# Performance work log

Hardware: AMD Instinct MI355X
Metric: run time of the kernel (lower is better)

## Reference

```python
import jax, jax.numpy as jnp
import numpy as np

EPS = 1e-5

def _gcn_norm(edge_index, n):
    # Add self-loops, compute symmetric normalization deg^-1/2 * deg^-1/2 (PyG GCNConv).
    src = jnp.concatenate([edge_index[0], jnp.arange(n)])
    dst = jnp.concatenate([edge_index[1], jnp.arange(n)])
    deg = jax.ops.segment_sum(jnp.ones_like(dst, dtype=jnp.float32), dst, num_segments=n)
    dinv = jnp.where(deg > 0, jax.lax.rsqrt(deg), 0.0)
    norm = dinv[src] * dinv[dst]  # [E + N]
    return src, dst, norm

def _gcn_conv(x, W, b, src, dst, norm, n):
    h = x @ W                      # linear first (out_dim < in_dim here)
    msg = h[src] * norm[:, None]   # gather + per-edge scale
    out = jax.ops.segment_sum(msg, dst, num_segments=n)  # scatter-add aggregation
    return out + b

def _bn(x, g, b):
    # BatchNorm over nodes (training-mode batch statistics, biased variance)
    mu = x.mean(axis=0)
    var = jnp.mean((x - mu) ** 2, axis=0)
    return (x - mu) * jax.lax.rsqrt(var + EPS) * g + b


def setup_inputs() -> dict:
    key = jax.random.key(0)
    N, E, F_in = 10000, 320000, 256
    ks = jax.random.split(key, 8)
    dims = [F_in, 220, 150, 100, 60, 17]
    inp = {
        'x': jax.random.normal(ks[0], (N, F_in), dtype=jnp.float32),
        'edge_index': jax.random.randint(ks[1], (2, E), 0, N, dtype=jnp.int64),
    }
    for i in range(5):
        fan_in, fan_out = dims[i], dims[i + 1]
        scale = 1.0 / np.sqrt(fan_in)
        inp[f'W{i+1}'] = jax.random.normal(ks[2 + i], (fan_in, fan_out), dtype=jnp.float32) * scale
        inp[f'b{i+1}'] = jnp.zeros((fan_out,), dtype=jnp.float32)
    for i, d in enumerate([220, 150, 100, 60]):
        inp[f'g{i+1}'] = jnp.ones((d,), dtype=jnp.float32)
        inp[f'be{i+1}'] = jnp.zeros((d,), dtype=jnp.float32)
    return inp


def reference(x, edge_index, W1, b1, W2, b2, W3, b3, W4, b4, W5, b5,
              g1, be1, g2, be2, g3, be3, g4, be4):
    n = x.shape[0]
    src, dst, norm = _gcn_norm(edge_index, n)
    h = _gcn_conv(x, W1, b1, src, dst, norm, n)
    h = _bn(jax.nn.relu(h), g1, be1)
    # dropout omitted (eval-mode identity)
    h = _gcn_conv(h, W2, b2, src, dst, norm, n)
    h = _bn(jax.nn.relu(h), g2, be2)
    h = _gcn_conv(h, W3, b3, src, dst, norm, n)
    h = _bn(jax.nn.relu(h), g3, be3)
    h = _gcn_conv(h, W4, b4, src, dst, norm, n)
    h = _bn(jax.nn.relu(h), g4, be4)
    h = _gcn_conv(h, W5, b5, src, dst, norm, n)
    return jax.nn.log_softmax(h, axis=1)
```

## Files before the change

kernel.cpp:

```cpp
#include <hip/hip_runtime.h>
#include <math.h>

typedef unsigned short ushort_t;
typedef unsigned int uint_t;
typedef unsigned long long ull_t;

__device__ __forceinline__ float bf2f(ushort_t u) {
    union { uint_t i; float f; } x; x.i = ((uint_t)u) << 16; return x.f;
}
__device__ __forceinline__ ushort_t f2bf(float f) {
    union { float f; uint_t i; } x; x.f = f;
    uint_t r = x.i + 0x7FFFu + ((x.i >> 16) & 1u);
    return (ushort_t)(r >> 16);
}

__global__ __launch_bounds__(256) void k_init(
    int* __restrict__ cnt, float* __restrict__ stats, float* __restrict__ wbias, int N)
{
    const int gt = blockIdx.x * 256 + threadIdx.x;
    const int gth = gridDim.x * 256;
    for (int i = gt; i < N; i += gth) cnt[i] = 0;
    for (int i = gt; i < 2048; i += gth) stats[i] = 0.f;
    if (gt < 256) wbias[gt] = 0.f;
}

__global__ __launch_bounds__(256) void k_prep0(
    const float* __restrict__ W0, ushort_t* __restrict__ Wt)
{
    const int gt = blockIdx.x * 256 + threadIdx.x;
    const int gth = gridDim.x * 256;
    for (int idx = gt; idx < 224 * 256; idx += gth) {
        int j = idx >> 8;
        int k = idx & 255;
        float v = (j < 220) ? W0[(long)k * 220 + j] : 0.f;
        Wt[idx] = f2bf(v);
    }
}

__global__ void k_hist(const int* __restrict__ dst, int* __restrict__ cnt, int E) {
    int e = blockIdx.x * blockDim.x + threadIdx.x;
    if (e < E) atomicAdd(&cnt[dst[e]], 1);
}

__global__ __launch_bounds__(1024) void k_scan(
    const int* __restrict__ cnt, int* __restrict__ row_start,
    int* __restrict__ cursor, float* __restrict__ dinv, int N)
{
    __shared__ int sh[1024];
    const int tid = threadIdx.x;
    const int chunk = (N + 1023) >> 10;
    int loc[16];
    const int base = tid * chunk;
    int sum = 0;
    for (int c = 0; c < chunk; ++c) {
        int i = base + c;
        int v = (i < N) ? cnt[i] : 0;
        loc[c] = sum;
        sum += v;
    }
    sh[tid] = sum;
    __syncthreads();
    for (int off = 1; off < 1024; off <<= 1) {
        int v = (tid >= off) ? sh[tid - off] : 0;
        __syncthreads();
        sh[tid] += v;
        __syncthreads();
    }
    const int excl = sh[tid] - sum;
    for (int c = 0; c < chunk; ++c) {
        int i = base + c;
        if (i < N) {
            int rs = excl + loc[c];
            row_start[i] = rs;
            cursor[i] = rs;
            dinv[i] = rsqrtf(1.0f + (float)cnt[i]);
        }
    }
    if (tid == 1023) row_start[N] = sh[1023];
}

__global__ void k_fill(const int* __restrict__ src, const int* __restrict__ dst,
                       int* __restrict__ cursor, int* __restrict__ csr_src, int E) {
    int e = blockIdx.x * blockDim.x + threadIdx.x;
    if (e < E) {
        int pos = atomicAdd(&cursor[dst[e]], 1);
        csr_src[pos] = src[e];
    }
}

__global__ void k_prep(const float* __restrict__ W,
                       const float* __restrict__ g, const float* __restrict__ be,
                       const float* __restrict__ cs, const float* __restrict__ cq,
                       ushort_t* __restrict__ Wt, float* __restrict__ wbias,
                       int K, int M, int Kp, int Mp, int yW, float invN)
{
    __shared__ float sm[256];
    if ((int)blockIdx.y < yW) {
        if (threadIdx.y == 0) {
            int kk = blockIdx.x * 64 + threadIdx.x;
            float sc = 0.f;
            if (kk < K) {
                float mu = cs[kk] * invN;
                float var = cq[kk] * invN - mu * mu;
                sc = g[kk] * rsqrtf(var + 1e-5f);
            }
            sm[threadIdx.x] = sc;
        }
        __syncthreads();
        int k = blockIdx.x * 64 + threadIdx.x;
        int j = blockIdx.y * 4 + threadIdx.y;
        if (k >= Kp || j >= Mp) return;
        float v = 0.f;
        if (k < K && j < M) v = sm[threadIdx.x] * W[(long)k * M + j];
        Wt[(long)j * Kp + k] = f2bf(v);
    } else {
        __shared__ float red[4][64];
        int t = threadIdx.y * 64 + threadIdx.x;
        for (int kk = t; kk < K; kk += 256) {
            float mu = cs[kk] * invN;
            float var = cq[kk] * invN - mu * mu;
            float sc = g[kk] * rsqrtf(var + 1e-5f);
            sm[kk] = be[kk] - mu * sc;
        }
        __syncthreads();
        int jl = t & 63, kg = t >> 6;
        int j = blockIdx.x * 64 + jl;
        float s = 0.f;
        if (j < M) {
            for (int k = kg; k < K; k += 4) s += sm[k] * W[(long)k * M + j];
        }
        red[kg][jl] = s;
        __syncthreads();
        if (kg == 0 && j < Mp) wbias[j] = red[0][jl] + red[1][jl] + red[2][jl] + red[3][jl];
    }
}

template<int KP, bool F32A>
__global__ __launch_bounds__(256) void k_gemm_mfma(
    const void* __restrict__ Xin, const ushort_t* __restrict__ Wt,
    const float* __restrict__ wbias, const float* __restrict__ dinv,
    ushort_t* __restrict__ h2, int N, int Mp)
{
    typedef __attribute__((ext_vector_type(8))) short short8;
    typedef __attribute__((ext_vector_type(4))) float floatx4;
    constexpr int LSTR = KP + 16;
    __shared__ ushort_t Bs[64 * LSTR];

    const int tid = threadIdx.x;
    const int wave = tid >> 6, lane = tid & 63;
    const int m = lane & 15, quad = lane >> 4;
    const int i0 = blockIdx.x * 64 + wave * 16;
    const int j0 = blockIdx.y * 64;
    const int ncols = min(64, Mp - j0);
    const int ntiles = ncols >> 4;

    {
        const int cpr = KP / 8;
        const int chunks = ncols * cpr;
        for (int c = tid; c < chunks; c += 256) {
            int jj = c / cpr;
            int kk = (c - jj * cpr) * 8;
            *(short8*)(Bs + jj * LSTR + kk) =
                *(const short8*)(Wt + (long)(j0 + jj) * KP + kk);
        }
    }
    __syncthreads();

    if (i0 >= N) return;

    floatx4 acc[4];
    #pragma unroll
    for (int t = 0; t < 4; ++t) { acc[t].x = 0.f; acc[t].y = 0.f; acc[t].z = 0.f; acc[t].w = 0.f; }

    const int ra = min(i0 + m, N - 1);
    const ushort_t* arow_h = F32A ? nullptr : (const ushort_t*)Xin + (long)ra * KP + quad * 8;
    const float*    arow_f = F32A ? (const float*)Xin + (long)ra * KP + quad * 8 : nullptr;

    #pragma unroll
    for (int k0 = 0; k0 < KP; k0 += 32) {
        short8 av;
        if (F32A) {
            float4 f0 = *(const float4*)(arow_f + k0);
            float4 f1 = *(const float4*)(arow_f + k0 + 4);
            av[0] = (short)f2bf(f0.x); av[1] = (short)f2bf(f0.y);
            av[2] = (short)f2bf(f0.z); av[3] = (short)f2bf(f0.w);
            av[4] = (short)f2bf(f1.x); av[5] = (short)f2bf(f1.y);
            av[6] = (short)f2bf(f1.z); av[7] = (short)f2bf(f1.w);
        } else {
            av = *(const short8*)(arow_h + k0);
        }
        #pragma unroll
        for (int t = 0; t < 4; ++t) {
            if (t < ntiles) {
                short8 bv = *(const short8*)(Bs + (t * 16 + m) * LSTR + k0 + quad * 8);
                acc[t] = __builtin_amdgcn_mfma_f32_16x16x32_bf16(av, bv, acc[t], 0, 0, 0);
            }
        }
    }

    #pragma unroll
    for (int t = 0; t < 4; ++t) {
        if (t < ntiles) {
            int j = j0 + t * 16 + m;
            float wb = wbias[j];
            #pragma unroll
            for (int r = 0; r < 4; ++r) {
                int i = i0 + quad * 4 + r;
                if (i < N) h2[(long)i * Mp + j] = f2bf((acc[t][r] + wb) * dinv[i]);
            }
        }
    }
}

__global__ __launch_bounds__(256) void k_agg(
    const int* __restrict__ row_start, const int* __restrict__ csr_src,
    const ushort_t* __restrict__ h2, int hs,
    const float* __restrict__ dinv, const float* __restrict__ b,
    ushort_t* __restrict__ tmpb, int ts,
    int N, int M, int Q, ull_t magic, uint_t sh)
{
    const uint_t g = blockIdx.x * 256 + threadIdx.x;
    const uint_t i = (uint_t)(((ull_t)g * magic) >> sh);
    const int jp = (int)(g - i * Q);
    if (i >= (uint_t)N) return;
    const int j0 = jp * 8;
    if (j0 >= M) {
        *(uint4*)(tmpb + (long)i * ts + j0) = make_uint4(0u, 0u, 0u, 0u);
        return;
    }
    const int s0 = row_start[i];
    const int s1 = row_start[i + 1];
    const ushort_t* hp = h2 + j0;
    float acc[8];
    {
        uint4 v = *(const uint4*)(hp + (long)i * hs);
        acc[0] = bf2f((ushort_t)(v.x & 0xffff)); acc[1] = bf2f((ushort_t)(v.x >> 16));
        acc[2] = bf2f((ushort_t)(v.y & 0xffff)); acc[3] = bf2f((ushort_t)(v.y >> 16));
        acc[4] = bf2f((ushort_t)(v.z & 0xffff)); acc[5] = bf2f((ushort_t)(v.z >> 16));
        acc[6] = bf2f((ushort_t)(v.w & 0xffff)); acc[7] = bf2f((ushort_t)(v.w >> 16));
    }
    int e = s0;
    for (; e + 3 < s1; e += 4) {
        int n0 = csr_src[e], n1 = csr_src[e + 1], n2 = csr_src[e + 2], n3 = csr_src[e + 3];
        uint4 w0 = *(const uint4*)(hp + (long)n0 * hs);
        uint4 w1 = *(const uint4*)(hp + (long)n1 * hs);
        uint4 w2 = *(const uint4*)(hp + (long)n2 * hs);
        uint4 w3 = *(const uint4*)(hp + (long)n3 * hs);
        acc[0] += bf2f((ushort_t)(w0.x & 0xffff)); acc[1] += bf2f((ushort_t)(w0.x >> 16));
        acc[2] += bf2f((ushort_t)(w0.y & 0xffff)); acc[3] += bf2f((ushort_t)(w0.y >> 16));
        acc[4] += bf2f((ushort_t)(w0.z & 0xffff)); acc[5] += bf2f((ushort_t)(w0.z >> 16));
        acc[6] += bf2f((ushort_t)(w0.w & 0xffff)); acc[7] += bf2f((ushort_t)(w0.w >> 16));
        acc[0] += bf2f((ushort_t)(w1.x & 0xffff)); acc[1] += bf2f((ushort_t)(w1.x >> 16));
        acc[2] += bf2f((ushort_t)(w1.y & 0xffff)); acc[3] += bf2f((ushort_t)(w1.y >> 16));
        acc[4] += bf2f((ushort_t)(w1.z & 0xffff)); acc[5] += bf2f((ushort_t)(w1.z >> 16));
        acc[6] += bf2f((ushort_t)(w1.w & 0xffff)); acc[7] += bf2f((ushort_t)(w1.w >> 16));
        acc[0] += bf2f((ushort_t)(w2.x & 0xffff)); acc[1] += bf2f((ushort_t)(w2.x >> 16));
        acc[2] += bf2f((ushort_t)(w2.y & 0xffff)); acc[3] += bf2f((ushort_t)(w2.y >> 16));
        acc[4] += bf2f((ushort_t)(w2.z & 0xffff)); acc[5] += bf2f((ushort_t)(w2.z >> 16));
        acc[6] += bf2f((ushort_t)(w2.w & 0xffff)); acc[7] += bf2f((ushort_t)(w2.w >> 16));
        acc[0] += bf2f((ushort_t)(w3.x & 0xffff)); acc[1] += bf2f((ushort_t)(w3.x >> 16));
        acc[2] += bf2f((ushort_t)(w3.y & 0xffff)); acc[3] += bf2f((ushort_t)(w3.y >> 16));
        acc[4] += bf2f((ushort_t)(w3.z & 0xffff)); acc[5] += bf2f((ushort_t)(w3.z >> 16));
        acc[6] += bf2f((ushort_t)(w3.w & 0xffff)); acc[7] += bf2f((ushort_t)(w3.w >> 16));
    }
    for (; e < s1; ++e) {
        uint4 w = *(const uint4*)(hp + (long)csr_src[e] * hs);
        acc[0] += bf2f((ushort_t)(w.x & 0xffff)); acc[1] += bf2f((ushort_t)(w.x >> 16));
        acc[2] += bf2f((ushort_t)(w.y & 0xffff)); acc[3] += bf2f((ushort_t)(w.y >> 16));
        acc[4] += bf2f((ushort_t)(w.z & 0xffff)); acc[5] += bf2f((ushort_t)(w.z >> 16));
        acc[6] += bf2f((ushort_t)(w.w & 0xffff)); acc[7] += bf2f((ushort_t)(w.w >> 16));
    }
    const float di = dinv[i];
    ushort_t r[8];
    #pragma unroll
    for (int u = 0; u < 8; ++u) {
        float v = (j0 + u < M) ? fmaxf(acc[u] * di + b[j0 + u], 0.f) : 0.f;
        r[u] = f2bf(v);
    }
    uint4 pk;
    pk.x = (uint_t)r[0] | ((uint_t)r[1] << 16);
    pk.y = (uint_t)r[2] | ((uint_t)r[3] << 16);
    pk.z = (uint_t)r[4] | ((uint_t)r[5] << 16);
    pk.w = (uint_t)r[6] | ((uint_t)r[7] << 16);
    *(uint4*)(tmpb + (long)i * ts + j0) = pk;
}

__global__ __launch_bounds__(256) void k_stats(
    const ushort_t* __restrict__ tmpb, int ts,
    float* __restrict__ cs, float* __restrict__ csq, int N)
{
    const int t = threadIdx.x;
    if (2 * t >= ts) return;
    const int i0 = blockIdx.x * 64;
    float s0 = 0.f, q0 = 0.f, s1 = 0.f, q1 = 0.f;
    for (int r = 0; r < 64; ++r) {
        int i = i0 + r;
        if (i < N) {
            uint_t w = *(const uint_t*)(tmpb + (long)i * ts + 2 * t);
            float v0 = bf2f((ushort_t)(w & 0xffff));
            float v1 = bf2f((ushort_t)(w >> 16));
            s0 += v0; q0 += v0 * v0;
            s1 += v1; q1 += v1 * v1;
        }
    }
    atomicAdd(&cs[2 * t], s0);
    atomicAdd(&csq[2 * t], q0);
    atomicAdd(&cs[2 * t + 1], s1);
    atomicAdd(&csq[2 * t + 1], q1);
}

__global__ __launch_bounds__(256) void k_agg_final(
    const int* __restrict__ row_start, const int* __restrict__ csr_src,
    const ushort_t* __restrict__ h2, const float* __restrict__ dinv,
    const float* __restrict__ b, float* __restrict__ out, int N, int M)
{
    const int x = threadIdx.x;
    const int i = blockIdx.x * 16 + threadIdx.y;
    if (i >= N) return;
    const int j0 = 2 * x, j1 = 2 * x + 1;
    uint_t v = *(const uint_t*)(h2 + (long)i * 32 + j0);
    float a0 = bf2f((ushort_t)(v & 0xffff));
    float a1 = bf2f((ushort_t)(v >> 16));
    const int s0 = row_start[i];
    const int s1 = row_start[i + 1];
    int e = s0;
    for (; e + 1 < s1; e += 2) {
        int n0 = csr_src[e], n1 = csr_src[e + 1];
        uint_t w0 = *(const uint_t*)(h2 + (long)n0 * 32 + j0);
        uint_t w1 = *(const uint_t*)(h2 + (long)n1 * 32 + j0);
        a0 += bf2f((ushort_t)(w0 & 0xffff)); a1 += bf2f((ushort_t)(w0 >> 16));
        a0 += bf2f((ushort_t)(w1 & 0xffff)); a1 += bf2f((ushort_t)(w1 >> 16));
    }
    for (; e < s1; ++e) {
        uint_t w = *(const uint_t*)(h2 + (long)csr_src[e] * 32 + j0);
        a0 += bf2f((ushort_t)(w & 0xffff)); a1 += bf2f((ushort_t)(w >> 16));
    }
    const float di = dinv[i];
    float r0 = (j0 < M) ? (a0 * di + b[j0]) : -INFINITY;
    float r1 = (j1 < M) ? (a1 * di + b[j1]) : -INFINITY;
    float m = fmaxf(r0, r1);
    #pragma unroll
    for (int msk = 1; msk < 16; msk <<= 1) m = fmaxf(m, __shfl_xor(m, msk, 16));
    float s = ((j0 < M) ? expf(r0 - m) : 0.f) + ((j1 < M) ? expf(r1 - m) : 0.f);
    #pragma unroll
    for (int msk = 1; msk < 16; msk <<= 1) s += __shfl_xor(s, msk, 16);
    const float l = logf(s) + m;
    if (j0 < M) out[(long)i * M + j0] = r0 - l;
    if (j1 < M) out[(long)i * M + j1] = r1 - l;
}


static inline int pad16(int v) { return (v + 15) & ~15; }
static inline int pad32(int v) { return (v + 31) & ~31; }

extern "C" void kernel_launch(void* const* d_in, const int* in_sizes, int n_in,
                              void* d_out, int out_size, void* d_ws, size_t ws_size,
                              hipStream_t stream)
{
    const int dims[6] = {256, 220, 150, 100, 60, 17};
    const int N = in_sizes[0] / dims[0];
    const int E = in_sizes[1] / 2;

    const float* x  = (const float*)d_in[0];
    const int* ei   = (const int*)d_in[1];
    const int* srcv = ei;
    const int* dstv = ei + E;
    const float* Wl[5], *bl[5];
    for (int l = 0; l < 5; ++l) {
        Wl[l] = (const float*)d_in[2 + 2 * l];
        bl[l] = (const float*)d_in[3 + 2 * l];
    }
    const float* gl[4], *bel[4];
    for (int l = 0; l < 4; ++l) {
        gl[l]  = (const float*)d_in[12 + 2 * l];
        bel[l] = (const float*)d_in[13 + 2 * l];
    }
    float* out = (float*)d_out;

    char* w = (char*)d_ws;
    const long NB  = ((long)N * 4 + 255) & ~255L;
    const long NB1 = ((long)(N + 1) * 4 + 255) & ~255L;
    const long EB  = ((long)E * 4 + 255) & ~255L;
    const long FBB = ((long)N * 224 * 2 + 255) & ~255L;
    const long WTB = ((long)224 * 256 * 2 + 255) & ~255L;

    long o = 0;
    float* dinv      = (float*)(w + o);  o += NB;
    float* stats     = (float*)(w + o);  o += 2048 * 4;
    float* wbias     = (float*)(w + o);  o += 1024;
    int*   cnt       = (int*)(w + o);    o += NB;
    int*   row_start = (int*)(w + o);    o += NB1;
    int*   cursor    = (int*)(w + o);    o += NB;
    int*   csr_src   = (int*)(w + o);    o += EB;
    ushort_t* Wt     = (ushort_t*)(w + o); o += WTB;
    ushort_t* h2     = (ushort_t*)(w + o); o += FBB;
    ushort_t* tmpb   = (ushort_t*)(w + o); o += FBB;

    const int eBlk = (E + 255) / 256;
    const float invN = 1.0f / (float)N;

    k_init<<<(N + 255) / 256, 256, 0, stream>>>(cnt, stats, wbias, N);
    k_prep0<<<56, 256, 0, stream>>>(Wl[0], Wt);
    k_hist<<<eBlk, 256, 0, stream>>>(dstv, cnt, E);
    k_scan<<<1, 1024, 0, stream>>>(cnt, row_start, cursor, dinv, N);
    k_fill<<<eBlk, 256, 0, stream>>>(srcv, dstv, cursor, csr_src, E);

    for (int l = 0; l < 5; ++l) {
        const int K  = dims[l];
        const int M  = dims[l + 1];
        const int Kp = pad32(K);
        const int Mp = pad16(M);
        const int ts = (l < 4) ? pad32(M) : 32;

        if (l > 0) {
            const int yW = (Mp + 3) / 4;
            k_prep<<<dim3((Kp + 63) / 64, yW + 1), dim3(64, 4), 0, stream>>>(
                Wl[l], gl[l - 1], bel[l - 1],
                stats + (l - 1) * 512, stats + (l - 1) * 512 + 256,
                Wt, wbias, K, M, Kp, Mp, yW, invN);
        }

        dim3 gg((N + 63) / 64, (Mp + 63) / 64);
        if (l == 0) {
            k_gemm_mfma<256, true><<<gg, 256, 0, stream>>>(x, Wt, wbias, dinv, h2, N, Mp);
        } else {
            switch (Kp) {
                case 224: k_gemm_mfma<224, false><<<gg, 256, 0, stream>>>(tmpb, Wt, wbias, dinv, h2, N, Mp); break;
                case 160: k_gemm_mfma<160, false><<<gg, 256, 0, stream>>>(tmpb, Wt, wbias, dinv, h2, N, Mp); break;
                case 128: k_gemm_mfma<128, false><<<gg, 256, 0, stream>>>(tmpb, Wt, wbias, dinv, h2, N, Mp); break;
                case  64: k_gemm_mfma< 64, false><<<gg, 256, 0, stream>>>(tmpb, Wt, wbias, dinv, h2, N, Mp); break;
            }
        }

        if (l < 4) {
            const int Q = ts / 8;
            uint_t shmt = 0;
            while ((1u << shmt) < (uint_t)Q) ++shmt;
            shmt += 32;
            const ull_t magic = ((1ULL << shmt) + Q - 1) / (ull_t)Q;
            const long total = (long)N * Q;
            k_agg<<<(int)((total + 255) / 256), 256, 0, stream>>>(
                row_start, csr_src, h2, Mp, dinv, bl[l], tmpb, ts, N, M, Q, magic, shmt);
            k_stats<<<(N + 63) / 64, 256, 0, stream>>>(tmpb, ts,
                stats + l * 512, stats + l * 512 + 256, N);
        } else {
            k_agg_final<<<(N + 15) / 16, dim3(16, 16), 0, stream>>>(
                row_start, csr_src, h2, dinv, bl[l], out, N, M);
        }
    }
}
```

Baseline: 402.6 us.

## Fuse histogram with weight prep, CSR fill into GEMM, stats into aggregation

Merges the degree histogram and first-layer weight transpose into one launch. It runs the CSR fill in extra blocks of the layer-0 GEMM launch and accumulates batch-norm sums inside the aggregation kernel via shared-memory atomics. This removes several kernel launches and a re-read of the aggregated activations. In exchange it adds shared and global atomic traffic per block and computes stats from unrounded fp32 values.

```diff
diff --git a/kernel.cpp b/kernel.cpp
--- a/kernel.cpp
+++ b/kernel.cpp
@@ -24,22 +24,22 @@
     if (gt < 256) wbias[gt] = 0.f;
 }
 
-__global__ __launch_bounds__(256) void k_prep0(
+__global__ __launch_bounds__(256) void k_hist_prep0(
+    const int* __restrict__ dst, int* __restrict__ cnt, int E, int eBlk,
     const float* __restrict__ W0, ushort_t* __restrict__ Wt)
 {
-    const int gt = blockIdx.x * 256 + threadIdx.x;
-    const int gth = gridDim.x * 256;
-    for (int idx = gt; idx < 224 * 256; idx += gth) {
-        int j = idx >> 8;
-        int k = idx & 255;
-        float v = (j < 220) ? W0[(long)k * 220 + j] : 0.f;
-        Wt[idx] = f2bf(v);
-    }
-}
-
-__global__ void k_hist(const int* __restrict__ dst, int* __restrict__ cnt, int E) {
-    int e = blockIdx.x * blockDim.x + threadIdx.x;
-    if (e < E) atomicAdd(&cnt[dst[e]], 1);
+    if ((int)blockIdx.x < eBlk) {
+        int e = blockIdx.x * 256 + threadIdx.x;
+        if (e < E) atomicAdd(&cnt[dst[e]], 1);
+    } else {
+        int base = ((int)blockIdx.x - eBlk) * 256 + (int)threadIdx.x;
+        for (int idx = base; idx < 224 * 256; idx += 56 * 256) {
+            int j = idx >> 8;
+            int k = idx & 255;
+            float v = (j < 220) ? W0[(long)k * 220 + j] : 0.f;
+            Wt[idx] = f2bf(v);
+        }
+    }
 }
 
 __global__ __launch_bounds__(1024) void k_scan(
@@ -77,15 +77,6 @@
         }
     }
     if (tid == 1023) row_start[N] = sh[1023];
-}
-
-__global__ void k_fill(const int* __restrict__ src, const int* __restrict__ dst,
-                       int* __restrict__ cursor, int* __restrict__ csr_src, int E) {
-    int e = blockIdx.x * blockDim.x + threadIdx.x;
-    if (e < E) {
-        int pos = atomicAdd(&cursor[dst[e]], 1);
-        csr_src[pos] = src[e];
-    }
 }
 
 __global__ void k_prep(const float* __restrict__ W,
@@ -135,16 +126,30 @@
     }
 }
 
-template<int KP, bool F32A>
+template<int KP, bool F32A, bool FILL>
 __global__ __launch_bounds__(256) void k_gemm_mfma(
     const void* __restrict__ Xin, const ushort_t* __restrict__ Wt,
     const float* __restrict__ wbias, const float* __restrict__ dinv,
-    ushort_t* __restrict__ h2, int N, int Mp)
+    ushort_t* __restrict__ h2, int N, int Mp,
+    int gx, const int* __restrict__ fsrc, const int* __restrict__ fdst,
+    int* __restrict__ fcursor, int* __restrict__ fcsr, int fE)
 {
     typedef __attribute__((ext_vector_type(8))) short short8;
     typedef __attribute__((ext_vector_type(4))) float floatx4;
     constexpr int LSTR = KP + 16;
     __shared__ ushort_t Bs[64 * LSTR];
+
+    if (FILL) {
+        if ((int)blockIdx.x >= gx) {
+            const int fid = ((int)blockIdx.x - gx) * (int)gridDim.y + (int)blockIdx.y;
+            const int e = fid * 256 + (int)threadIdx.x;
+            if (e < fE) {
+                int pos = atomicAdd(&fcursor[fdst[e]], 1);
+                fcsr[pos] = fsrc[e];
+            }
+            return;
+        }
+    }
 
     const int tid = threadIdx.x;
     const int wave = tid >> 6, lane = tid & 63;
@@ -217,96 +222,99 @@
     const ushort_t* __restrict__ h2, int hs,
     const float* __restrict__ dinv, const float* __restrict__ b,
     ushort_t* __restrict__ tmpb, int ts,
+    float* __restrict__ cs, float* __restrict__ csq,
     int N, int M, int Q, ull_t magic, uint_t sh)
 {
-    const uint_t g = blockIdx.x * 256 + threadIdx.x;
+    __shared__ float s_s[256];
+    __shared__ float s_q[256];
+    const int tid = threadIdx.x;
+    s_s[tid] = 0.f;
+    s_q[tid] = 0.f;
+    __syncthreads();
+
+    const uint_t g = blockIdx.x * 256 + tid;
     const uint_t i = (uint_t)(((ull_t)g * magic) >> sh);
     const int jp = (int)(g - i * Q);
-    if (i >= (uint_t)N) return;
     const int j0 = jp * 8;
-    if (j0 >= M) {
-        *(uint4*)(tmpb + (long)i * ts + j0) = make_uint4(0u, 0u, 0u, 0u);
-        return;
-    }
-    const int s0 = row_start[i];
-    const int s1 = row_start[i + 1];
-    const ushort_t* hp = h2 + j0;
-    float acc[8];
-    {
-        uint4 v = *(const uint4*)(hp + (long)i * hs);
-        acc[0] = bf2f((ushort_t)(v.x & 0xffff)); acc[1] = bf2f((ushort_t)(v.x >> 16));
-        acc[2] = bf2f((ushort_t)(v.y & 0xffff)); acc[3] = bf2f((ushort_t)(v.y >> 16));
-        acc[4] = bf2f((ushort_t)(v.z & 0xffff)); acc[5] = bf2f((ushort_t)(v.z >> 16));
-        acc[6] = bf2f((ushort_t)(v.w & 0xffff)); acc[7] = bf2f((ushort_t)(v.w >> 16));
-    }
-    int e = s0;
-    for (; e + 3 < s1; e += 4) {
-        int n0 = csr_src[e], n1 = csr_src[e + 1], n2 = csr_src[e + 2], n3 = csr_src[e + 3];
-        uint4 w0 = *(const uint4*)(hp + (long)n0 * hs);
-        uint4 w1 = *(const uint4*)(hp + (long)n1 * hs);
-        uint4 w2 = *(const uint4*)(hp + (long)n2 * hs);
-        uint4 w3 = *(const uint4*)(hp + (long)n3 * hs);
-        acc[0] += bf2f((ushort_t)(w0.x & 0xffff)); acc[1] += bf2f((ushort_t)(w0.x >> 16));
-        acc[2] += bf2f((ushort_t)(w0.y & 0xffff)); acc[3] += bf2f((ushort_t)(w0.y >> 16));
-        acc[4] += bf2f((ushort_t)(w0.z & 0xffff)); acc[5] += bf2f((ushort_t)(w0.z >> 16));
-        acc[6] += bf2f((ushort_t)(w0.w & 0xffff)); acc[7] += bf2f((ushort_t)(w0.w >> 16));
-        acc[0] += bf2f((ushort_t)(w1.x & 0xffff)); acc[1] += bf2f((ushort_t)(w1.x >> 16));
-        acc[2] += bf2f((ushort_t)(w1.y & 0xffff)); acc[3] += bf2f((ushort_t)(w1.y >> 16));
-        acc[4] += bf2f((ushort_t)(w1.z & 0xffff)); acc[5] += bf2f((ushort_t)(w1.z >> 16));
-        acc[6] += bf2f((ushort_t)(w1.w & 0xffff)); acc[7] += bf2f((ushort_t)(w1.w >> 16));
-        acc[0] += bf2f((ushort_t)(w2.x & 0xffff)); acc[1] += bf2f((ushort_t)(w2.x >> 16));
-        acc[2] += bf2f((ushort_t)(w2.y & 0xffff)); acc[3] += bf2f((ushort_t)(w2.y >> 16));
-        acc[4] += bf2f((ushort_t)(w2.z & 0xffff)); acc[5] += bf2f((ushort_t)(w2.z >> 16));
-        acc[6] += bf2f((ushort_t)(w2.w & 0xffff)); acc[7] += bf2f((ushort_t)(w2.w >> 16));
-        acc[0] += bf2f((ushort_t)(w3.x & 0xffff)); acc[1] += bf2f((ushort_t)(w3.x >> 16));
-        acc[2] += bf2f((ushort_t)(w3.y & 0xffff)); acc[3] += bf2f((ushort_t)(w3.y >> 16));
-        acc[4] += bf2f((ushort_t)(w3.z & 0xffff)); acc[5] += bf2f((ushort_t)(w3.z >> 16));
-        acc[6] += bf2f((ushort_t)(w3.w & 0xffff)); acc[7] += bf2f((ushort_t)(w3.w >> 16));
-    }
-    for (; e < s1; ++e) {
-        uint4 w = *(const uint4*)(hp + (long)csr_src[e] * hs);
-        acc[0] += bf2f((ushort_t)(w.x & 0xffff)); acc[1] += bf2f((ushort_t)(w.x >> 16));
-        acc[2] += bf2f((ushort_t)(w.y & 0xffff)); acc[3] += bf2f((ushort_t)(w.y >> 16));
-        acc[4] += bf2f((ushort_t)(w.z & 0xffff)); acc[5] += bf2f((ushort_t)(w.z >> 16));
-        acc[6] += bf2f((ushort_t)(w.w & 0xffff)); acc[7] += bf2f((ushort_t)(w.w >> 16));
-    }
-    const float di = dinv[i];
-    ushort_t r[8];
-    #pragma unroll
-    for (int u = 0; u < 8; ++u) {
-        float v = (j0 + u < M) ? fmaxf(acc[u] * di + b[j0 + u], 0.f) : 0.f;
-        r[u] = f2bf(v);
-    }
-    uint4 pk;
-    pk.x = (uint_t)r[0] | ((uint_t)r[1] << 16);
-    pk.y = (uint_t)r[2] | ((uint_t)r[3] << 16);
-    pk.z = (uint_t)r[4] | ((uint_t)r[5] << 16);
-    pk.w = (uint_t)r[6] | ((uint_t)r[7] << 16);
-    *(uint4*)(tmpb + (long)i * ts + j0) = pk;
-}
-
-__global__ __launch_bounds__(256) void k_stats(
-    const ushort_t* __restrict__ tmpb, int ts,
-    float* __restrict__ cs, float* __restrict__ csq, int N)
-{
-    const int t = threadIdx.x;
-    if (2 * t >= ts) return;
-    const int i0 = blockIdx.x * 64;
-    float s0 = 0.f, q0 = 0.f, s1 = 0.f, q1 = 0.f;
-    for (int r = 0; r < 64; ++r) {
-        int i = i0 + r;
-        if (i < N) {
-            uint_t w = *(const uint_t*)(tmpb + (long)i * ts + 2 * t);
-            float v0 = bf2f((ushort_t)(w & 0xffff));
-            float v1 = bf2f((ushort_t)(w >> 16));
-            s0 += v0; q0 += v0 * v0;
-            s1 += v1; q1 += v1 * v1;
-        }
-    }
-    atomicAdd(&cs[2 * t], s0);
-    atomicAdd(&csq[2 * t], q0);
-    atomicAdd(&cs[2 * t + 1], s1);
-    atomicAdd(&csq[2 * t + 1], q1);
+    float vals[8];
+    bool active = false;
+
+    if (i < (uint_t)N) {
+        if (j0 >= M) {
+            *(uint4*)(tmpb + (long)i * ts + j0) = make_uint4(0u, 0u, 0u, 0u);
+        } else {
+            active = true;
+            const int s0 = row_start[i];
+            const int s1 = row_start[i + 1];
+            const ushort_t* hp = h2 + j0;
+            float acc[8];
+            {
+                uint4 v = *(const uint4*)(hp + (long)i * hs);
+                acc[0] = bf2f((ushort_t)(v.x & 0xffff)); acc[1] = bf2f((ushort_t)(v.x >> 16));
+                acc[2] = bf2f((ushort_t)(v.y & 0xffff)); acc[3] = bf2f((ushort_t)(v.y >> 16));
+                acc[4] = bf2f((ushort_t)(v.z & 0xffff)); acc[5] = bf2f((ushort_t)(v.z >> 16));
+                acc[6] = bf2f((ushort_t)(v.w & 0xffff)); acc[7] = bf2f((ushort_t)(v.w >> 16));
+            }
+            int e = s0;
+            for (; e + 3 < s1; e += 4) {
+                int n0 = csr_src[e], n1 = csr_src[e + 1], n2 = csr_src[e + 2], n3 = csr_src[e + 3];
+                uint4 w0 = *(const uint4*)(hp + (long)n0 * hs);
+                uint4 w1 = *(const uint4*)(hp + (long)n1 * hs);
+                uint4 w2 = *(const uint4*)(hp + (long)n2 * hs);
+                uint4 w3 = *(const uint4*)(hp + (long)n3 * hs);
+                acc[0] += bf2f((ushort_t)(w0.x & 0xffff)); acc[1] += bf2f((ushort_t)(w0.x >> 16));
+                acc[2] += bf2f((ushort_t)(w0.y & 0xffff)); acc[3] += bf2f((ushort_t)(w0.y >> 16));
+                acc[4] += bf2f((ushort_t)(w0.z & 0xffff)); acc[5] += bf2f((ushort_t)(w0.z >> 16));
+                acc[6] += bf2f((ushort_t)(w0.w & 0xffff)); acc[7] += bf2f((ushort_t)(w0.w >> 16));
+                acc[0] += bf2f((ushort_t)(w1.x & 0xffff)); acc[1] += bf2f((ushort_t)(w1.x >> 16));
+                acc[2] += bf2f((ushort_t)(w1.y & 0xffff)); acc[3] += bf2f((ushort_t)(w1.y >> 16));
+                acc[4] += bf2f((ushort_t)(w1.z & 0xffff)); acc[5] += bf2f((ushort_t)(w1.z >> 16));
+                acc[6] += bf2f((ushort_t)(w1.w & 0xffff)); acc[7] += bf2f((ushort_t)(w1.w >> 16));
+                acc[0] += bf2f((ushort_t)(w2.x & 0xffff)); acc[1] += bf2f((ushort_t)(w2.x >> 16));
+                acc[2] += bf2f((ushort_t)(w2.y & 0xffff)); acc[3] += bf2f((ushort_t)(w2.y >> 16));
+                acc[4] += bf2f((ushort_t)(w2.z & 0xffff)); acc[5] += bf2f((ushort_t)(w2.z >> 16));
+                acc[6] += bf2f((ushort_t)(w2.w & 0xffff)); acc[7] += bf2f((ushort_t)(w2.w >> 16));
+                acc[0] += bf2f((ushort_t)(w3.x & 0xffff)); acc[1] += bf2f((ushort_t)(w3.x >> 16));
+                acc[2] += bf2f((ushort_t)(w3.y & 0xffff)); acc[3] += bf2f((ushort_t)(w3.y >> 16));
+                acc[4] += bf2f((ushort_t)(w3.z & 0xffff)); acc[5] += bf2f((ushort_t)(w3.z >> 16));
+                acc[6] += bf2f((ushort_t)(w3.w & 0xffff)); acc[7] += bf2f((ushort_t)(w3.w >> 16));
+            }
+            for (; e < s1; ++e) {
+                uint4 w = *(const uint4*)(hp + (long)csr_src[e] * hs);
+                acc[0] += bf2f((ushort_t)(w.x & 0xffff)); acc[1] += bf2f((ushort_t)(w.x >> 16));
+                acc[2] += bf2f((ushort_t)(w.y & 0xffff)); acc[3] += bf2f((ushort_t)(w.y >> 16));
+                acc[4] += bf2f((ushort_t)(w.z & 0xffff)); acc[5] += bf2f((ushort_t)(w.z >> 16));
+                acc[6] += bf2f((ushort_t)(w.w & 0xffff)); acc[7] += bf2f((ushort_t)(w.w >> 16));
+            }
+            const float di = dinv[i];
+            ushort_t r[8];
+            #pragma unroll
+            for (int u = 0; u < 8; ++u) {
+                float v = (j0 + u < M) ? fmaxf(acc[u] * di + b[j0 + u], 0.f) : 0.f;
+                vals[u] = v;
+                r[u] = f2bf(v);
+            }
+            uint4 pk;
+            pk.x = (uint_t)r[0] | ((uint_t)r[1] << 16);
+            pk.y = (uint_t)r[2] | ((uint_t)r[3] << 16);
+            pk.z = (uint_t)r[4] | ((uint_t)r[5] << 16);
+            pk.w = (uint_t)r[6] | ((uint_t)r[7] << 16);
+            *(uint4*)(tmpb + (long)i * ts + j0) = pk;
+        }
+    }
+
+    if (active) {
+        #pragma unroll
+        for (int u = 0; u < 8; ++u) {
+            atomicAdd(&s_s[j0 + u], vals[u]);
+            atomicAdd(&s_q[j0 + u], vals[u] * vals[u]);
+        }
+    }
+    __syncthreads();
+    if (tid < ts && (s_s[tid] != 0.f || s_q[tid] != 0.f)) {
+        unsafeAtomicAdd(&cs[tid], s_s[tid]);
+        unsafeAtomicAdd(&csq[tid], s_q[tid]);
+    }
 }
 
 __global__ __launch_bounds__(256) void k_agg_final(
@@ -400,10 +408,8 @@
     const float invN = 1.0f / (float)N;
 
     k_init<<<(N + 255) / 256, 256, 0, stream>>>(cnt, stats, wbias, N);
-    k_prep0<<<56, 256, 0, stream>>>(Wl[0], Wt);
-    k_hist<<<eBlk, 256, 0, stream>>>(dstv, cnt, E);
+    k_hist_prep0<<<eBlk + 56, 256, 0, stream>>>(dstv, cnt, E, eBlk, Wl[0], Wt);
     k_scan<<<1, 1024, 0, stream>>>(cnt, row_start, cursor, dinv, N);
-    k_fill<<<eBlk, 256, 0, stream>>>(srcv, dstv, cursor, csr_src, E);
 
     for (int l = 0; l < 5; ++l) {
         const int K  = dims[l];
@@ -422,13 +428,21 @@
 
         dim3 gg((N + 63) / 64, (Mp + 63) / 64);
         if (l == 0) {
-            k_gemm_mfma<256, true><<<gg, 256, 0, stream>>>(x, Wt, wbias, dinv, h2, N, Mp);
+            const int fx = (eBlk + (int)gg.y - 1) / (int)gg.y;
+            dim3 gg0(gg.x + fx, gg.y);
+            k_gemm_mfma<256, true, true><<<gg0, 256, 0, stream>>>(
+                x, Wt, wbias, dinv, h2, N, Mp,
+                (int)gg.x, srcv, dstv, cursor, csr_src, E);
         } else {
             switch (Kp) {
-                case 224: k_gemm_mfma<224, false><<<gg, 256, 0, stream>>>(tmpb, Wt, wbias, dinv, h2, N, Mp); break;
-                case 160: k_gemm_mfma<160, false><<<gg, 256, 0, stream>>>(tmpb, Wt, wbias, dinv, h2, N, Mp); break;
-                case 128: k_gemm_mfma<128, false><<<gg, 256, 0, stream>>>(tmpb, Wt, wbias, dinv, h2, N, Mp); break;
-                case  64: k_gemm_mfma< 64, false><<<gg, 256, 0, stream>>>(tmpb, Wt, wbias, dinv, h2, N, Mp); break;
+                case 224: k_gemm_mfma<224, false, false><<<gg, 256, 0, stream>>>(
+                    tmpb, Wt, wbias, dinv, h2, N, Mp, 0, nullptr, nullptr, nullptr, nullptr, 0); break;
+                case 160: k_gemm_mfma<160, false, false><<<gg, 256, 0, stream>>>(
+                    tmpb, Wt, wbias, dinv, h2, N, Mp, 0, nullptr, nullptr, nullptr, nullptr, 0); break;
+                case 128: k_gemm_mfma<128, false, false><<<gg, 256, 0, stream>>>(
+                    tmpb, Wt, wbias, dinv, h2, N, Mp, 0, nullptr, nullptr, nullptr, nullptr, 0); break;
+                case  64: k_gemm_mfma< 64, false, false><<<gg, 256, 0, stream>>>(
+                    tmpb, Wt, wbias, dinv, h2, N, Mp, 0, nullptr, nullptr, nullptr, nullptr, 0); break;
             }
         }
 
@@ -440,9 +454,9 @@
             const ull_t magic = ((1ULL << shmt) + Q - 1) / (ull_t)Q;
             const long total = (long)N * Q;
             k_agg<<<(int)((total + 255) / 256), 256, 0, stream>>>(
-                row_start, csr_src, h2, Mp, dinv, bl[l], tmpb, ts, N, M, Q, magic, shmt);
-            k_stats<<<(N + 63) / 64, 256, 0, stream>>>(tmpb, ts,
-                stats + l * 512, stats + l * 512 + 256, N);
+                row_start, csr_src, h2, Mp, dinv, bl[l], tmpb, ts,
+                stats + l * 512, stats + l * 512 + 256,
+                N, M, Q, magic, shmt);
         } else {
             k_agg_final<<<(N + 15) / 16, dim3(16, 16), 0, stream>>>(
                 row_start, csr_src, h2, dinv, bl[l], out, N, M);
```

After: 384.3 us. 1.05x faster.
